# Kernel tuning notes

Hardware: AMD Instinct MI355X
Metric: run time of the kernel (lower is better)

## Reference

```python
import jax, jax.numpy as jnp
import numpy as np

B, N, F, UNITS = 8, 2048, 64, 64

def setup_inputs() -> dict:
    key = jax.random.key(0)
    ks = jax.random.split(key, 7)
    inputs = jax.random.normal(ks[0], (B, N, F), dtype=jnp.float32)
    Dynamic_L = jax.random.normal(ks[1], (B, N, N), dtype=jnp.float32)
    W = jax.random.uniform(ks[2], (B, N, N, 3), dtype=jnp.float32)
    Geo = jax.random.normal(ks[3], (N, N), dtype=jnp.float32)
    KL = jax.random.normal(ks[4], (N, N), dtype=jnp.float32)
    # Dense(Units, tanh) params (glorot-ish scale)
    Wd = jax.random.normal(ks[5], (F, UNITS), dtype=jnp.float32) / np.sqrt(F)
    bd = jnp.zeros((UNITS,), dtype=jnp.float32)
    return {"inputs": inputs, "Dynamic_L": Dynamic_L, "W": W,
            "Geo": Geo, "KL": KL, "Wd": Wd, "bd": bd}

def reference(inputs, Dynamic_L, W, Geo, KL, Wd, bd):
    # Weighted fusion of three N x N matrices; Geo/KL broadcast over batch.
    Fusion = Dynamic_L * W[..., 0] + Geo[None] * W[..., 1] + KL[None] * W[..., 2]  # [B,N,N]
    Fusion = jax.nn.softmax(Fusion, axis=-1)
    G1 = jnp.einsum('bnm,bmf->bnf', Fusion, inputs)  # graph matmul [B,N,F]
    return jnp.tanh(G1 @ Wd + bd)  # Dense(Units, tanh) -> [B,N,UNITS]
```

## Files before the change

### kernel.cpp

```cpp
#include <hip/hip_runtime.h>
#include <hip/hip_fp16.h>

#define Nn 2048
#define Ff 64
#define Uu 64
#define NT 256
#define NCH 4

typedef _Float16 f16x4 __attribute__((ext_vector_type(4)));
typedef _Float16 f16x8 __attribute__((ext_vector_type(8)));
typedef float    f32x4 __attribute__((ext_vector_type(4)));

#define MFMA32(a,b,c) __builtin_amdgcn_mfma_f32_16x16x32_f16(a,b,c,0,0,0)
#define G1S 68

__global__ __launch_bounds__(256) void transposeX(const float* __restrict__ X,
                                                  _Float16* __restrict__ Xt) {
    __shared__ _Float16 tile[64][65];
    const int b = blockIdx.x, kt = blockIdx.y;
    #pragma unroll
    for (int i = 0; i < 16; ++i) {
        int e  = i * 256 + threadIdx.x;
        int kk = e >> 6, ff = e & 63;
        tile[ff][kk] = (_Float16)X[((size_t)b * Nn + kt * 64 + kk) * Ff + ff];
    }
    __syncthreads();
    #pragma unroll
    for (int i = 0; i < 16; ++i) {
        int e  = i * 256 + threadIdx.x;
        int ff = e >> 6, kk = e & 63;
        Xt[((size_t)b * Ff + ff) * Nn + kt * 64 + kk] = tile[ff][kk];
    }
}

#define ISSUE_HR(Vd,Vw0,Vw1,Vw2,Vg,Vk, C, HR) {               \
    const int _rr = (HR) >> 1;                                \
    const int _m  = ((C) << 9) + (((HR) & 1) << 8) + (lane << 2); \
    const size_t _o = (size_t)_rr * Nn + _m;                  \
    Vd  = *(const float4*)(dR + _o);                          \
    Vw0 = *(const float4*)(wR + 3 * _o);                      \
    Vw1 = *(const float4*)(wR + 3 * _o + 4);                  \
    Vw2 = *(const float4*)(wR + 3 * _o + 8);                  \
    Vg  = *(const float4*)(gR + _o);                          \
    Vk  = *(const float4*)(kR + _o);                          \
}

#define CONSUME_HR(Vd,Vw0,Vw1,Vw2,Vg,Vk, BUF, HR) {                           \
    const int _rr = (HR) >> 1;                                                \
    const int _tr = row0 + _rr;                                               \
    float _e0 = __expf(fminf(Vd.x*Vw0.x + Vg.x*Vw0.y + Vk.x*Vw0.z, 11.f));    \
    float _e1 = __expf(fminf(Vd.y*Vw0.w + Vg.y*Vw1.x + Vk.y*Vw1.y, 11.f));    \
    float _e2 = __expf(fminf(Vd.z*Vw1.z + Vg.z*Vw1.w + Vk.z*Vw2.x, 11.f));    \
    float _e3 = __expf(fminf(Vd.w*Vw2.y + Vg.w*Vw2.z + Vk.w*Vw2.w, 11.f));    \
    f16x4 _h = {(_Float16)_e0, (_Float16)_e1, (_Float16)_e2, (_Float16)_e3};  \
    rs[_rr] += (float)_h[0] + (float)_h[1] + (float)_h[2] + (float)_h[3];     \
    const int _ba = _tr*1024 + (((HR)&1) << 9) + (lane << 3);                 \
    *(f16x4*)((char*)(BUF) + (_ba ^ ((_tr & 7) << 4))) = _h;                  \
}

#define STAGE_CHUNK(BUF, C) {                          \
    ISSUE_HR(Ad,Aw0,Aw1,Aw2,Ag,Ak, C, 0);              \
    ISSUE_HR(Bd,Bw0,Bw1,Bw2,Bg,Bk, C, 1);              \
    CONSUME_HR(Ad,Aw0,Aw1,Aw2,Ag,Ak, BUF, 0);          \
    ISSUE_HR(Ad,Aw0,Aw1,Aw2,Ag,Ak, C, 2);              \
    CONSUME_HR(Bd,Bw0,Bw1,Bw2,Bg,Bk, BUF, 1);          \
    ISSUE_HR(Bd,Bw0,Bw1,Bw2,Bg,Bk, C, 3);              \
    CONSUME_HR(Ad,Aw0,Aw1,Aw2,Ag,Ak, BUF, 2);          \
    ISSUE_HR(Ad,Aw0,Aw1,Aw2,Ag,Ak, C, 4);              \
    CONSUME_HR(Bd,Bw0,Bw1,Bw2,Bg,Bk, BUF, 3);          \
    ISSUE_HR(Bd,Bw0,Bw1,Bw2,Bg,Bk, C, 5);              \
    CONSUME_HR(Ad,Aw0,Aw1,Aw2,Ag,Ak, BUF, 4);          \
    ISSUE_HR(Ad,Aw0,Aw1,Aw2,Ag,Ak, C, 6);              \
    CONSUME_HR(Bd,Bw0,Bw1,Bw2,Bg,Bk, BUF, 5);          \
    ISSUE_HR(Bd,Bw0,Bw1,Bw2,Bg,Bk, C, 7);              \
    CONSUME_HR(Ad,Aw0,Aw1,Aw2,Ag,Ak, BUF, 6);          \
    CONSUME_HR(Bd,Bw0,Bw1,Bw2,Bg,Bk, BUF, 7);          \
}

#define MFMA_PHASE(BUFC, XC) {                                                \
    f16x8 p0 = *(const f16x8*)((XC));                                         \
    f16x8 p1 = *(const f16x8*)((XC) + 32);                                    \
    f16x8 p2 = *(const f16x8*)((XC) + 64);                                    \
    f16x8 p3 = *(const f16x8*)((XC) + 96);                                    \
    f16x8 p4 = *(const f16x8*)((XC) + 128);                                   \
    f16x8 p5 = *(const f16x8*)((XC) + 160);                                   \
    f16x8 p6 = *(const f16x8*)((XC) + 192);                                   \
    f16x8 p7 = *(const f16x8*)((XC) + 224);                                   \
    _Pragma("unroll")                                                         \
    for (int kk = 0; kk < 8; ++kk) {                                          \
        const int aa = r * 1024 + kk * 64 + kg * 16;                          \
        f16x8 af = *(const f16x8*)((BUFC) + (aa ^ ((r & 7) << 4)));           \
        f16x8 bv = (kk==0)?p0:(kk==1)?p1:(kk==2)?p2:(kk==3)?p3:               \
                   (kk==4)?p4:(kk==5)?p5:(kk==6)?p6:p7;                       \
        acc = MFMA32(af, bv, acc);                                            \
    }                                                                         \
    p0 = *(const f16x8*)((XC) + 256);                                         \
    p1 = *(const f16x8*)((XC) + 288);                                         \
    p2 = *(const f16x8*)((XC) + 320);                                         \
    p3 = *(const f16x8*)((XC) + 352);                                         \
    p4 = *(const f16x8*)((XC) + 384);                                         \
    p5 = *(const f16x8*)((XC) + 416);                                         \
    p6 = *(const f16x8*)((XC) + 448);                                         \
    p7 = *(const f16x8*)((XC) + 480);                                         \
    _Pragma("unroll")                                                         \
    for (int kk = 0; kk < 8; ++kk) {                                          \
        const int aa = r * 1024 + (kk + 8) * 64 + kg * 16;                    \
        f16x8 af = *(const f16x8*)((BUFC) + (aa ^ ((r & 7) << 4)));           \
        f16x8 bv = (kk==0)?p0:(kk==1)?p1:(kk==2)?p2:(kk==3)?p3:               \
                   (kk==4)?p4:(kk==5)?p5:(kk==6)?p6:p7;                       \
        acc = MFMA32(af, bv, acc);                                            \
    }                                                                         \
}

__global__ __launch_bounds__(NT, 4) void fused_gcn(
    const _Float16* __restrict__ Xt,
    const float* __restrict__ Dyn,
    const float* __restrict__ Wf,
    const float* __restrict__ Geo,
    const float* __restrict__ KLm,
    const float* __restrict__ Wd,
    const float* __restrict__ bdv,
    float* __restrict__ out)
{
    __shared__ _Float16 Pb[2][16 * 512];
    __shared__ float wsumS[16];
    __shared__ float invS[16];

    const int t    = threadIdx.x;
    const int lane = t & 63;
    const int wid  = t >> 6;
    const int r    = lane & 15;
    const int kg   = lane >> 4;
    const int b    = blockIdx.x >> 7;
    const int n0   = (blockIdx.x & 127) << 4;
    const int row0 = wid << 2;

    const float* dR = Dyn + ((size_t)b * Nn + n0 + row0) * Nn;
    const float* wR = Wf  + ((size_t)b * Nn + n0 + row0) * (size_t)Nn * 3;
    const float* gR = Geo + (size_t)(n0 + row0) * Nn;
    const float* kR = KLm + (size_t)(n0 + row0) * Nn;
    const _Float16* XtB = Xt + (size_t)b * Ff * Nn;
    const _Float16* xw  = XtB + (size_t)(wid * 16 + r) * Nn + (kg << 3);

    f32x4 acc = {0.f, 0.f, 0.f, 0.f};
    float rs[4] = {0.f, 0.f, 0.f, 0.f};
    float4 Ad, Aw0, Aw1, Aw2, Ag, Ak;
    float4 Bd, Bw0, Bw1, Bw2, Bg, Bk;

    STAGE_CHUNK(&Pb[0][0], 0);
    __syncthreads();

    #pragma unroll 1
    for (int c = 0; c < NCH; ++c) {
        const char* bufc = (const char*)&Pb[c & 1][0];
        MFMA_PHASE(bufc, xw + (c << 9));
        if (c + 1 < NCH) {
            _Float16* bufn = &Pb[(c + 1) & 1][0];
            STAGE_CHUNK(bufn, c + 1);
        }
        __syncthreads();
    }

    #pragma unroll
    for (int i = 0; i < 4; ++i) {
        float v = rs[i];
        v += __shfl_xor(v, 1, 64);  v += __shfl_xor(v, 2, 64);
        v += __shfl_xor(v, 4, 64);  v += __shfl_xor(v, 8, 64);
        v += __shfl_xor(v, 16, 64); v += __shfl_xor(v, 32, 64);
        rs[i] = v;
    }
    if (lane == 0) {
        wsumS[row0 + 0] = rs[0]; wsumS[row0 + 1] = rs[1];
        wsumS[row0 + 2] = rs[2]; wsumS[row0 + 3] = rs[3];
    }
    __syncthreads();
    if (t < 16) invS[t] = 1.0f / wsumS[t];
    __syncthreads();

    float* g1 = (float*)&Pb[0][0];
    #pragma unroll
    for (int i = 0; i < 4; ++i) {
        const int ro = (kg << 2) + i;
        g1[ro * G1S + (wid << 4) + r] = acc[i] * invS[ro];
    }
    __syncthreads();

    const float* g1r = g1 + row0 * G1S;
    float o0 = bdv[lane], o1 = o0, o2 = o0, o3 = o0;
    #pragma unroll 4
    for (int f = 0; f < Ff; ++f) {
        float wdv = Wd[f * Uu + lane];
        o0 += g1r[f]           * wdv;
        o1 += g1r[G1S + f]     * wdv;
        o2 += g1r[2 * G1S + f] * wdv;
        o3 += g1r[3 * G1S + f] * wdv;
    }
    float oo[4] = {o0, o1, o2, o3};
    #pragma unroll
    for (int i = 0; i < 4; ++i) {
        float x  = fminf(fmaxf(oo[i], -15.f), 15.f);
        float ex = __expf(2.f * x);
        out[((size_t)b * Nn + n0 + row0 + i) * Uu + lane] = (ex - 1.f) / (ex + 1.f);
    }
}

extern "C" void kernel_launch(void* const* d_in, const int* in_sizes, int n_in,
                              void* d_out, int out_size, void* d_ws, size_t ws_size,
                              hipStream_t stream) {
    const float* X   = (const float*)d_in[0];
    const float* Dyn = (const float*)d_in[1];
    const float* Wf  = (const float*)d_in[2];
    const float* Geo = (const float*)d_in[3];
    const float* KLm = (const float*)d_in[4];
    const float* Wd  = (const float*)d_in[5];
    const float* bdv = (const float*)d_in[6];
    float* out = (float*)d_out;

    _Float16* Xt = (_Float16*)d_ws;
    transposeX<<<dim3(8, Nn / 64), dim3(256), 0, stream>>>(X, Xt);
    fused_gcn<<<dim3(8 * (Nn / 16)), dim3(NT), 0, stream>>>(
        Xt, Dyn, Wf, Geo, KLm, Wd, bdv, out);
}
```

Baseline: 129.5 us.

## Warp-specialize fused GCN into producer softmax waves and consumer MFMA waves

Result: slower. 158.7 us (+22.5%).

```diff
diff --git a/kernel.cpp b/kernel.cpp
--- a/kernel.cpp
+++ b/kernel.cpp
@@ -5,7 +5,8 @@
 #define Ff 64
 #define Uu 64
 #define NT 256
-#define NCH 4
+#define CW 256
+#define NCH 8
 
 typedef _Float16 f16x4 __attribute__((ext_vector_type(4)));
 typedef _Float16 f16x8 __attribute__((ext_vector_type(8)));
@@ -33,83 +34,59 @@
     }
 }
 
-#define ISSUE_HR(Vd,Vw0,Vw1,Vw2,Vg,Vk, C, HR) {               \
-    const int _rr = (HR) >> 1;                                \
-    const int _m  = ((C) << 9) + (((HR) & 1) << 8) + (lane << 2); \
-    const size_t _o = (size_t)_rr * Nn + _m;                  \
-    Vd  = *(const float4*)(dR + _o);                          \
-    Vw0 = *(const float4*)(wR + 3 * _o);                      \
-    Vw1 = *(const float4*)(wR + 3 * _o + 4);                  \
-    Vw2 = *(const float4*)(wR + 3 * _o + 8);                  \
-    Vg  = *(const float4*)(gR + _o);                          \
-    Vk  = *(const float4*)(kR + _o);                          \
-}
-
-#define CONSUME_HR(Vd,Vw0,Vw1,Vw2,Vg,Vk, BUF, HR) {                           \
-    const int _rr = (HR) >> 1;                                                \
-    const int _tr = row0 + _rr;                                               \
+#define ISSUE_U(Vd,Vw0,Vw1,Vw2,Vg,Vk, C, U) {                 \
+    const size_t _o = (size_t)(U) * Nn + (size_t)(C) * CW + (lane << 2); \
+    Vd  = *(const float4*)(dP + _o);                          \
+    Vw0 = *(const float4*)(wP + 3 * _o);                      \
+    Vw1 = *(const float4*)(wP + 3 * _o + 4);                  \
+    Vw2 = *(const float4*)(wP + 3 * _o + 8);                  \
+    Vg  = *(const float4*)(gP + _o);                          \
+    Vk  = *(const float4*)(kP + _o);                          \
+}
+
+#define CONSUME_U(Vd,Vw0,Vw1,Vw2,Vg,Vk, BUF, U) {                             \
     float _e0 = __expf(fminf(Vd.x*Vw0.x + Vg.x*Vw0.y + Vk.x*Vw0.z, 11.f));    \
     float _e1 = __expf(fminf(Vd.y*Vw0.w + Vg.y*Vw1.x + Vk.y*Vw1.y, 11.f));    \
     float _e2 = __expf(fminf(Vd.z*Vw1.z + Vg.z*Vw1.w + Vk.z*Vw2.x, 11.f));    \
     float _e3 = __expf(fminf(Vd.w*Vw2.y + Vg.w*Vw2.z + Vk.w*Vw2.w, 11.f));    \
     f16x4 _h = {(_Float16)_e0, (_Float16)_e1, (_Float16)_e2, (_Float16)_e3};  \
-    rs[_rr] += (float)_h[0] + (float)_h[1] + (float)_h[2] + (float)_h[3];     \
-    const int _ba = _tr*1024 + (((HR)&1) << 9) + (lane << 3);                 \
-    *(f16x4*)((char*)(BUF) + (_ba ^ ((_tr & 7) << 4))) = _h;                  \
-}
-
-#define STAGE_CHUNK(BUF, C) {                          \
-    ISSUE_HR(Ad,Aw0,Aw1,Aw2,Ag,Ak, C, 0);              \
-    ISSUE_HR(Bd,Bw0,Bw1,Bw2,Bg,Bk, C, 1);              \
-    CONSUME_HR(Ad,Aw0,Aw1,Aw2,Ag,Ak, BUF, 0);          \
-    ISSUE_HR(Ad,Aw0,Aw1,Aw2,Ag,Ak, C, 2);              \
-    CONSUME_HR(Bd,Bw0,Bw1,Bw2,Bg,Bk, BUF, 1);          \
-    ISSUE_HR(Bd,Bw0,Bw1,Bw2,Bg,Bk, C, 3);              \
-    CONSUME_HR(Ad,Aw0,Aw1,Aw2,Ag,Ak, BUF, 2);          \
-    ISSUE_HR(Ad,Aw0,Aw1,Aw2,Ag,Ak, C, 4);              \
-    CONSUME_HR(Bd,Bw0,Bw1,Bw2,Bg,Bk, BUF, 3);          \
-    ISSUE_HR(Bd,Bw0,Bw1,Bw2,Bg,Bk, C, 5);              \
-    CONSUME_HR(Ad,Aw0,Aw1,Aw2,Ag,Ak, BUF, 4);          \
-    ISSUE_HR(Ad,Aw0,Aw1,Aw2,Ag,Ak, C, 6);              \
-    CONSUME_HR(Bd,Bw0,Bw1,Bw2,Bg,Bk, BUF, 5);          \
-    ISSUE_HR(Bd,Bw0,Bw1,Bw2,Bg,Bk, C, 7);              \
-    CONSUME_HR(Ad,Aw0,Aw1,Aw2,Ag,Ak, BUF, 6);          \
-    CONSUME_HR(Bd,Bw0,Bw1,Bw2,Bg,Bk, BUF, 7);          \
-}
-
-#define MFMA_PHASE(BUFC, XC) {                                                \
-    f16x8 p0 = *(const f16x8*)((XC));                                         \
-    f16x8 p1 = *(const f16x8*)((XC) + 32);                                    \
-    f16x8 p2 = *(const f16x8*)((XC) + 64);                                    \
-    f16x8 p3 = *(const f16x8*)((XC) + 96);                                    \
-    f16x8 p4 = *(const f16x8*)((XC) + 128);                                   \
-    f16x8 p5 = *(const f16x8*)((XC) + 160);                                   \
-    f16x8 p6 = *(const f16x8*)((XC) + 192);                                   \
-    f16x8 p7 = *(const f16x8*)((XC) + 224);                                   \
-    _Pragma("unroll")                                                         \
-    for (int kk = 0; kk < 8; ++kk) {                                          \
-        const int aa = r * 1024 + kk * 64 + kg * 16;                          \
-        f16x8 af = *(const f16x8*)((BUFC) + (aa ^ ((r & 7) << 4)));           \
-        f16x8 bv = (kk==0)?p0:(kk==1)?p1:(kk==2)?p2:(kk==3)?p3:               \
-                   (kk==4)?p4:(kk==5)?p5:(kk==6)?p6:p7;                       \
-        acc = MFMA32(af, bv, acc);                                            \
-    }                                                                         \
-    p0 = *(const f16x8*)((XC) + 256);                                         \
-    p1 = *(const f16x8*)((XC) + 288);                                         \
-    p2 = *(const f16x8*)((XC) + 320);                                         \
-    p3 = *(const f16x8*)((XC) + 352);                                         \
-    p4 = *(const f16x8*)((XC) + 384);                                         \
-    p5 = *(const f16x8*)((XC) + 416);                                         \
-    p6 = *(const f16x8*)((XC) + 448);                                         \
-    p7 = *(const f16x8*)((XC) + 480);                                         \
-    _Pragma("unroll")                                                         \
-    for (int kk = 0; kk < 8; ++kk) {                                          \
-        const int aa = r * 1024 + (kk + 8) * 64 + kg * 16;                    \
-        f16x8 af = *(const f16x8*)((BUFC) + (aa ^ ((r & 7) << 4)));           \
-        f16x8 bv = (kk==0)?p0:(kk==1)?p1:(kk==2)?p2:(kk==3)?p3:               \
-                   (kk==4)?p4:(kk==5)?p5:(kk==6)?p6:p7;                       \
-        acc = MFMA32(af, bv, acc);                                            \
-    }                                                                         \
+    rs[U] += (float)_h[0] + (float)_h[1] + (float)_h[2] + (float)_h[3];       \
+    const int _ba = (p8 + (U)) * 512 + (lane << 3);                           \
+    *(f16x4*)((char*)(BUF) + (_ba ^ (((U) & 7) << 4))) = _h;                  \
+}
+
+#define STAGE_BODY(BUF, C, PRE) {                          \
+    CONSUME_U(Ad,Aw0,Aw1,Aw2,Ag,Ak, BUF, 0);               \
+    ISSUE_U(Ad,Aw0,Aw1,Aw2,Ag,Ak, C, 2);                   \
+    CONSUME_U(Bd,Bw0,Bw1,Bw2,Bg,Bk, BUF, 1);               \
+    ISSUE_U(Bd,Bw0,Bw1,Bw2,Bg,Bk, C, 3);                   \
+    CONSUME_U(Ad,Aw0,Aw1,Aw2,Ag,Ak, BUF, 2);               \
+    ISSUE_U(Ad,Aw0,Aw1,Aw2,Ag,Ak, C, 4);                   \
+    CONSUME_U(Bd,Bw0,Bw1,Bw2,Bg,Bk, BUF, 3);               \
+    ISSUE_U(Bd,Bw0,Bw1,Bw2,Bg,Bk, C, 5);                   \
+    CONSUME_U(Ad,Aw0,Aw1,Aw2,Ag,Ak, BUF, 4);               \
+    ISSUE_U(Ad,Aw0,Aw1,Aw2,Ag,Ak, C, 6);                   \
+    CONSUME_U(Bd,Bw0,Bw1,Bw2,Bg,Bk, BUF, 5);               \
+    ISSUE_U(Bd,Bw0,Bw1,Bw2,Bg,Bk, C, 7);                   \
+    CONSUME_U(Ad,Aw0,Aw1,Aw2,Ag,Ak, BUF, 6);               \
+    if (PRE) { ISSUE_U(Ad,Aw0,Aw1,Aw2,Ag,Ak, (C)+1, 0); }  \
+    CONSUME_U(Bd,Bw0,Bw1,Bw2,Bg,Bk, BUF, 7);               \
+    if (PRE) { ISSUE_U(Bd,Bw0,Bw1,Bw2,Bg,Bk, (C)+1, 1); }  \
+}
+
+#define MFMA_CHUNK(BUF, C) {                                        \
+    const char* _bc = (const char*)(BUF);                           \
+    const _Float16* _x0 = xB0 + (size_t)(C) * CW;                   \
+    const _Float16* _x1 = xB1 + (size_t)(C) * CW;                   \
+    _Pragma("unroll")                                               \
+    for (int kk = 0; kk < 8; ++kk) {                                \
+        const int aa = r * 512 + kk * 64 + kg * 16;                 \
+        f16x8 af = *(const f16x8*)(_bc + (aa ^ ((r & 7) << 4)));    \
+        f16x8 b0 = *(const f16x8*)(_x0 + kk * 32);                  \
+        f16x8 b1 = *(const f16x8*)(_x1 + kk * 32);                  \
+        acc0 = MFMA32(af, b0, acc0);                                \
+        acc1 = MFMA32(af, b1, acc1);                                \
+    }                                                               \
 }
 
 __global__ __launch_bounds__(NT, 4) void fused_gcn(
@@ -122,9 +99,10 @@
     const float* __restrict__ bdv,
     float* __restrict__ out)
 {
-    __shared__ _Float16 Pb[2][16 * 512];
+    __shared__ _Float16 Pb[2][16 * CW];
     __shared__ float wsumS[16];
     __shared__ float invS[16];
+    __shared__ float g1[16 * G1S];
 
     const int t    = threadIdx.x;
     const int lane = t & 63;
@@ -133,58 +111,65 @@
     const int kg   = lane >> 4;
     const int b    = blockIdx.x >> 7;
     const int n0   = (blockIdx.x & 127) << 4;
-    const int row0 = wid << 2;
-
-    const float* dR = Dyn + ((size_t)b * Nn + n0 + row0) * Nn;
-    const float* wR = Wf  + ((size_t)b * Nn + n0 + row0) * (size_t)Nn * 3;
-    const float* gR = Geo + (size_t)(n0 + row0) * Nn;
-    const float* kR = KLm + (size_t)(n0 + row0) * Nn;
-    const _Float16* XtB = Xt + (size_t)b * Ff * Nn;
-    const _Float16* xw  = XtB + (size_t)(wid * 16 + r) * Nn + (kg << 3);
-
-    f32x4 acc = {0.f, 0.f, 0.f, 0.f};
-    float rs[4] = {0.f, 0.f, 0.f, 0.f};
+
+    const int p  = wid & 1;
+    const int p8 = p << 3;
+    const float* dP = Dyn + ((size_t)b * Nn + n0 + p8) * Nn;
+    const float* wP = Wf  + ((size_t)b * Nn + n0 + p8) * (size_t)Nn * 3;
+    const float* gP = Geo + (size_t)(n0 + p8) * Nn;
+    const float* kP = KLm + (size_t)(n0 + p8) * Nn;
+
+    const int cw = wid & 1;
+    const _Float16* xB0 = Xt + (size_t)b * Ff * Nn
+                        + (size_t)((cw * 2) * 16 + r) * Nn + (kg << 3);
+    const _Float16* xB1 = xB0 + (size_t)16 * Nn;
+
+    float rs[8] = {0.f,0.f,0.f,0.f,0.f,0.f,0.f,0.f};
+    f32x4 acc0 = {0.f,0.f,0.f,0.f}, acc1 = {0.f,0.f,0.f,0.f};
     float4 Ad, Aw0, Aw1, Aw2, Ag, Ak;
     float4 Bd, Bw0, Bw1, Bw2, Bg, Bk;
 
-    STAGE_CHUNK(&Pb[0][0], 0);
-    __syncthreads();
+    if (wid < 2) {
+        ISSUE_U(Ad,Aw0,Aw1,Aw2,Ag,Ak, 0, 0);
+        ISSUE_U(Bd,Bw0,Bw1,Bw2,Bg,Bk, 0, 1);
+    }
 
     #pragma unroll 1
-    for (int c = 0; c < NCH; ++c) {
-        const char* bufc = (const char*)&Pb[c & 1][0];
-        MFMA_PHASE(bufc, xw + (c << 9));
-        if (c + 1 < NCH) {
-            _Float16* bufn = &Pb[(c + 1) & 1][0];
-            STAGE_CHUNK(bufn, c + 1);
+    for (int it = 0; it < NCH + 1; ++it) {
+        if (wid < 2) {
+            if (it < NCH) STAGE_BODY(&Pb[it & 1][0], it, (it + 1 < NCH));
+        } else {
+            if (it > 0) MFMA_CHUNK(&Pb[(it - 1) & 1][0], it - 1);
         }
         __syncthreads();
     }
 
-    #pragma unroll
-    for (int i = 0; i < 4; ++i) {
-        float v = rs[i];
-        v += __shfl_xor(v, 1, 64);  v += __shfl_xor(v, 2, 64);
-        v += __shfl_xor(v, 4, 64);  v += __shfl_xor(v, 8, 64);
-        v += __shfl_xor(v, 16, 64); v += __shfl_xor(v, 32, 64);
-        rs[i] = v;
-    }
-    if (lane == 0) {
-        wsumS[row0 + 0] = rs[0]; wsumS[row0 + 1] = rs[1];
-        wsumS[row0 + 2] = rs[2]; wsumS[row0 + 3] = rs[3];
+    if (wid < 2) {
+        #pragma unroll
+        for (int u = 0; u < 8; ++u) {
+            float v = rs[u];
+            v += __shfl_xor(v, 1, 64);  v += __shfl_xor(v, 2, 64);
+            v += __shfl_xor(v, 4, 64);  v += __shfl_xor(v, 8, 64);
+            v += __shfl_xor(v, 16, 64); v += __shfl_xor(v, 32, 64);
+            if (lane == 0) wsumS[p8 + u] = v;
+        }
     }
     __syncthreads();
     if (t < 16) invS[t] = 1.0f / wsumS[t];
     __syncthreads();
 
-    float* g1 = (float*)&Pb[0][0];
-    #pragma unroll
-    for (int i = 0; i < 4; ++i) {
-        const int ro = (kg << 2) + i;
-        g1[ro * G1S + (wid << 4) + r] = acc[i] * invS[ro];
-    }
-    __syncthreads();
-
+    if (wid >= 2) {
+        #pragma unroll
+        for (int i = 0; i < 4; ++i) {
+            const int ro = (kg << 2) + i;
+            const float inv = invS[ro];
+            g1[ro * G1S + (cw * 2) * 16 + r]       = acc0[i] * inv;
+            g1[ro * G1S + (cw * 2 + 1) * 16 + r]   = acc1[i] * inv;
+        }
+    }
+    __syncthreads();
+
+    const int row0 = wid << 2;
     const float* g1r = g1 + row0 * G1S;
     float o0 = bdv[lane], o1 = o0, o2 = o0, o3 = o0;
     #pragma unroll 4
```

## Process two batches per block to share Geo/KL row loads

Applied to the files above, without the earlier changes.

Measured after the change: 130.9 us. About the same (+1.1%).

```diff
diff --git a/kernel.cpp b/kernel.cpp
--- a/kernel.cpp
+++ b/kernel.cpp
@@ -6,13 +6,20 @@
 #define Uu 64
 #define NT 256
 #define NCH 4
+#define G1S 68
 
 typedef _Float16 f16x4 __attribute__((ext_vector_type(4)));
 typedef _Float16 f16x8 __attribute__((ext_vector_type(8)));
 typedef float    f32x4 __attribute__((ext_vector_type(4)));
 
 #define MFMA32(a,b,c) __builtin_amdgcn_mfma_f32_16x16x32_f16(a,b,c,0,0,0)
-#define G1S 68
+
+#define OPB   0
+#define OG1A  65536
+#define OG1B  69888
+#define OWS   74240
+#define OINV  74368
+#define SMSZ  74496
 
 __global__ __launch_bounds__(256) void transposeX(const float* __restrict__ X,
                                                   _Float16* __restrict__ Xt) {
@@ -33,51 +40,63 @@
     }
 }
 
-#define ISSUE_HR(Vd,Vw0,Vw1,Vw2,Vg,Vk, C, HR) {               \
-    const int _rr = (HR) >> 1;                                \
-    const int _m  = ((C) << 9) + (((HR) & 1) << 8) + (lane << 2); \
-    const size_t _o = (size_t)_rr * Nn + _m;                  \
-    Vd  = *(const float4*)(dR + _o);                          \
-    Vw0 = *(const float4*)(wR + 3 * _o);                      \
-    Vw1 = *(const float4*)(wR + 3 * _o + 4);                  \
-    Vw2 = *(const float4*)(wR + 3 * _o + 8);                  \
-    Vg  = *(const float4*)(gR + _o);                          \
-    Vk  = *(const float4*)(kR + _o);                          \
-}
-
-#define CONSUME_HR(Vd,Vw0,Vw1,Vw2,Vg,Vk, BUF, HR) {                           \
-    const int _rr = (HR) >> 1;                                                \
-    const int _tr = row0 + _rr;                                               \
-    float _e0 = __expf(fminf(Vd.x*Vw0.x + Vg.x*Vw0.y + Vk.x*Vw0.z, 11.f));    \
-    float _e1 = __expf(fminf(Vd.y*Vw0.w + Vg.y*Vw1.x + Vk.y*Vw1.y, 11.f));    \
-    float _e2 = __expf(fminf(Vd.z*Vw1.z + Vg.z*Vw1.w + Vk.z*Vw2.x, 11.f));    \
-    float _e3 = __expf(fminf(Vd.w*Vw2.y + Vg.w*Vw2.z + Vk.w*Vw2.w, 11.f));    \
-    f16x4 _h = {(_Float16)_e0, (_Float16)_e1, (_Float16)_e2, (_Float16)_e3};  \
-    rs[_rr] += (float)_h[0] + (float)_h[1] + (float)_h[2] + (float)_h[3];     \
-    const int _ba = _tr*1024 + (((HR)&1) << 9) + (lane << 3);                 \
-    *(f16x4*)((char*)(BUF) + (_ba ^ ((_tr & 7) << 4))) = _h;                  \
-}
-
-#define STAGE_CHUNK(BUF, C) {                          \
-    ISSUE_HR(Ad,Aw0,Aw1,Aw2,Ag,Ak, C, 0);              \
-    ISSUE_HR(Bd,Bw0,Bw1,Bw2,Bg,Bk, C, 1);              \
-    CONSUME_HR(Ad,Aw0,Aw1,Aw2,Ag,Ak, BUF, 0);          \
-    ISSUE_HR(Ad,Aw0,Aw1,Aw2,Ag,Ak, C, 2);              \
-    CONSUME_HR(Bd,Bw0,Bw1,Bw2,Bg,Bk, BUF, 1);          \
-    ISSUE_HR(Bd,Bw0,Bw1,Bw2,Bg,Bk, C, 3);              \
-    CONSUME_HR(Ad,Aw0,Aw1,Aw2,Ag,Ak, BUF, 2);          \
-    ISSUE_HR(Ad,Aw0,Aw1,Aw2,Ag,Ak, C, 4);              \
-    CONSUME_HR(Bd,Bw0,Bw1,Bw2,Bg,Bk, BUF, 3);          \
-    ISSUE_HR(Bd,Bw0,Bw1,Bw2,Bg,Bk, C, 5);              \
-    CONSUME_HR(Ad,Aw0,Aw1,Aw2,Ag,Ak, BUF, 4);          \
-    ISSUE_HR(Ad,Aw0,Aw1,Aw2,Ag,Ak, C, 6);              \
-    CONSUME_HR(Bd,Bw0,Bw1,Bw2,Bg,Bk, BUF, 5);          \
-    ISSUE_HR(Bd,Bw0,Bw1,Bw2,Bg,Bk, C, 7);              \
-    CONSUME_HR(Ad,Aw0,Aw1,Aw2,Ag,Ak, BUF, 6);          \
-    CONSUME_HR(Bd,Bw0,Bw1,Bw2,Bg,Bk, BUF, 7);          \
-}
-
-#define MFMA_PHASE(BUFC, XC) {                                                \
+#define ISSUE2(d0v,d1v,gv,kv,w00,w01,w02,w10,w11,w12, C, HR) {      \
+    const int _rr = (HR) >> 1;                                      \
+    const size_t _o = (size_t)_rr * Nn + ((size_t)(C) << 9)         \
+                    + (((HR) & 1) << 8) + (lane << 2);              \
+    d0v = *(const float4*)(dR0 + _o);                               \
+    d1v = *(const float4*)(dR1 + _o);                               \
+    gv  = *(const float4*)(gR + _o);                                \
+    kv  = *(const float4*)(kR + _o);                                \
+    w00 = *(const float4*)(wR0 + 3 * _o);                           \
+    w01 = *(const float4*)(wR0 + 3 * _o + 4);                       \
+    w02 = *(const float4*)(wR0 + 3 * _o + 8);                       \
+    w10 = *(const float4*)(wR1 + 3 * _o);                           \
+    w11 = *(const float4*)(wR1 + 3 * _o + 4);                       \
+    w12 = *(const float4*)(wR1 + 3 * _o + 8);                       \
+}
+
+#define CONSUME2(d0v,d1v,gv,kv,w00,w01,w02,w10,w11,w12, P0B,P1B, HR) {          \
+    const int _rr = (HR) >> 1;                                                  \
+    const int _tr = row0 + _rr;                                                 \
+    float a0 = __expf(fminf(d0v.x*w00.x + gv.x*w00.y + kv.x*w00.z, 11.f));      \
+    float a1 = __expf(fminf(d0v.y*w00.w + gv.y*w01.x + kv.y*w01.y, 11.f));      \
+    float a2 = __expf(fminf(d0v.z*w01.z + gv.z*w01.w + kv.z*w02.x, 11.f));      \
+    float a3 = __expf(fminf(d0v.w*w02.y + gv.w*w02.z + kv.w*w02.w, 11.f));      \
+    float c0 = __expf(fminf(d1v.x*w10.x + gv.x*w10.y + kv.x*w10.z, 11.f));      \
+    float c1 = __expf(fminf(d1v.y*w10.w + gv.y*w11.x + kv.y*w11.y, 11.f));      \
+    float c2 = __expf(fminf(d1v.z*w11.z + gv.z*w11.w + kv.z*w12.x, 11.f));      \
+    float c3 = __expf(fminf(d1v.w*w12.y + gv.w*w12.z + kv.w*w12.w, 11.f));      \
+    f16x4 h0 = {(_Float16)a0, (_Float16)a1, (_Float16)a2, (_Float16)a3};        \
+    f16x4 h1 = {(_Float16)c0, (_Float16)c1, (_Float16)c2, (_Float16)c3};        \
+    rs0[_rr] += (float)h0[0] + (float)h0[1] + (float)h0[2] + (float)h0[3];      \
+    rs1[_rr] += (float)h1[0] + (float)h1[1] + (float)h1[2] + (float)h1[3];      \
+    const int _ba = (_tr * 1024 + (((HR) & 1) << 9) + (lane << 3))              \
+                    ^ ((_tr & 7) << 4);                                         \
+    *(f16x4*)((P0B) + _ba) = h0;                                                \
+    *(f16x4*)((P1B) + _ba) = h1;                                                \
+}
+
+#define STAGE_CHUNK2(P0B, P1B, C) {                                              \
+    ISSUE2(Ad0,Ad1,Agv,Akv,Aw00,Aw01,Aw02,Aw10,Aw11,Aw12, C, 0);                 \
+    ISSUE2(Bd0,Bd1,Bgv,Bkv,Bw00,Bw01,Bw02,Bw10,Bw11,Bw12, C, 1);                 \
+    CONSUME2(Ad0,Ad1,Agv,Akv,Aw00,Aw01,Aw02,Aw10,Aw11,Aw12, P0B,P1B, 0);         \
+    ISSUE2(Ad0,Ad1,Agv,Akv,Aw00,Aw01,Aw02,Aw10,Aw11,Aw12, C, 2);                 \
+    CONSUME2(Bd0,Bd1,Bgv,Bkv,Bw00,Bw01,Bw02,Bw10,Bw11,Bw12, P0B,P1B, 1);         \
+    ISSUE2(Bd0,Bd1,Bgv,Bkv,Bw00,Bw01,Bw02,Bw10,Bw11,Bw12, C, 3);                 \
+    CONSUME2(Ad0,Ad1,Agv,Akv,Aw00,Aw01,Aw02,Aw10,Aw11,Aw12, P0B,P1B, 2);         \
+    ISSUE2(Ad0,Ad1,Agv,Akv,Aw00,Aw01,Aw02,Aw10,Aw11,Aw12, C, 4);                 \
+    CONSUME2(Bd0,Bd1,Bgv,Bkv,Bw00,Bw01,Bw02,Bw10,Bw11,Bw12, P0B,P1B, 3);         \
+    ISSUE2(Bd0,Bd1,Bgv,Bkv,Bw00,Bw01,Bw02,Bw10,Bw11,Bw12, C, 5);                 \
+    CONSUME2(Ad0,Ad1,Agv,Akv,Aw00,Aw01,Aw02,Aw10,Aw11,Aw12, P0B,P1B, 4);         \
+    ISSUE2(Ad0,Ad1,Agv,Akv,Aw00,Aw01,Aw02,Aw10,Aw11,Aw12, C, 6);                 \
+    CONSUME2(Bd0,Bd1,Bgv,Bkv,Bw00,Bw01,Bw02,Bw10,Bw11,Bw12, P0B,P1B, 5);         \
+    ISSUE2(Bd0,Bd1,Bgv,Bkv,Bw00,Bw01,Bw02,Bw10,Bw11,Bw12, C, 7);                 \
+    CONSUME2(Ad0,Ad1,Agv,Akv,Aw00,Aw01,Aw02,Aw10,Aw11,Aw12, P0B,P1B, 6);         \
+    CONSUME2(Bd0,Bd1,Bgv,Bkv,Bw00,Bw01,Bw02,Bw10,Bw11,Bw12, P0B,P1B, 7);         \
+}
+
+#define MFMA_PHASE2(PBUF, XC, ACC) {                                          \
     f16x8 p0 = *(const f16x8*)((XC));                                         \
     f16x8 p1 = *(const f16x8*)((XC) + 32);                                    \
     f16x8 p2 = *(const f16x8*)((XC) + 64);                                    \
@@ -89,10 +108,10 @@
     _Pragma("unroll")                                                         \
     for (int kk = 0; kk < 8; ++kk) {                                          \
         const int aa = r * 1024 + kk * 64 + kg * 16;                          \
-        f16x8 af = *(const f16x8*)((BUFC) + (aa ^ ((r & 7) << 4)));           \
+        f16x8 af = *(const f16x8*)((PBUF) + (aa ^ ((r & 7) << 4)));           \
         f16x8 bv = (kk==0)?p0:(kk==1)?p1:(kk==2)?p2:(kk==3)?p3:               \
                    (kk==4)?p4:(kk==5)?p5:(kk==6)?p6:p7;                       \
-        acc = MFMA32(af, bv, acc);                                            \
+        ACC = MFMA32(af, bv, ACC);                                            \
     }                                                                         \
     p0 = *(const f16x8*)((XC) + 256);                                         \
     p1 = *(const f16x8*)((XC) + 288);                                         \
@@ -105,14 +124,14 @@
     _Pragma("unroll")                                                         \
     for (int kk = 0; kk < 8; ++kk) {                                          \
         const int aa = r * 1024 + (kk + 8) * 64 + kg * 16;                    \
-        f16x8 af = *(const f16x8*)((BUFC) + (aa ^ ((r & 7) << 4)));           \
+        f16x8 af = *(const f16x8*)((PBUF) + (aa ^ ((r & 7) << 4)));           \
         f16x8 bv = (kk==0)?p0:(kk==1)?p1:(kk==2)?p2:(kk==3)?p3:               \
                    (kk==4)?p4:(kk==5)?p5:(kk==6)?p6:p7;                       \
-        acc = MFMA32(af, bv, acc);                                            \
+        ACC = MFMA32(af, bv, ACC);                                            \
     }                                                                         \
 }
 
-__global__ __launch_bounds__(NT, 4) void fused_gcn(
+__global__ __launch_bounds__(NT, 2) void fused_gcn(
     const _Float16* __restrict__ Xt,
     const float* __restrict__ Dyn,
     const float* __restrict__ Wf,
@@ -122,85 +141,100 @@
     const float* __restrict__ bdv,
     float* __restrict__ out)
 {
-    __shared__ _Float16 Pb[2][16 * 512];
-    __shared__ float wsumS[16];
-    __shared__ float invS[16];
+    __shared__ __align__(16) char SM[SMSZ];
 
     const int t    = threadIdx.x;
     const int lane = t & 63;
     const int wid  = t >> 6;
     const int r    = lane & 15;
     const int kg   = lane >> 4;
-    const int b    = blockIdx.x >> 7;
-    const int n0   = (blockIdx.x & 127) << 4;
+    const int rg   = blockIdx.x & 127;
+    const int pp   = blockIdx.x >> 7;
+    const int n0   = rg << 4;
+    const int b0   = pp * 2, b1 = pp * 2 + 1;
     const int row0 = wid << 2;
 
-    const float* dR = Dyn + ((size_t)b * Nn + n0 + row0) * Nn;
-    const float* wR = Wf  + ((size_t)b * Nn + n0 + row0) * (size_t)Nn * 3;
-    const float* gR = Geo + (size_t)(n0 + row0) * Nn;
-    const float* kR = KLm + (size_t)(n0 + row0) * Nn;
-    const _Float16* XtB = Xt + (size_t)b * Ff * Nn;
-    const _Float16* xw  = XtB + (size_t)(wid * 16 + r) * Nn + (kg << 3);
-
-    f32x4 acc = {0.f, 0.f, 0.f, 0.f};
-    float rs[4] = {0.f, 0.f, 0.f, 0.f};
-    float4 Ad, Aw0, Aw1, Aw2, Ag, Ak;
-    float4 Bd, Bw0, Bw1, Bw2, Bg, Bk;
-
-    STAGE_CHUNK(&Pb[0][0], 0);
+    const float* dR0 = Dyn + ((size_t)b0 * Nn + n0 + row0) * Nn;
+    const float* dR1 = Dyn + ((size_t)b1 * Nn + n0 + row0) * Nn;
+    const float* wR0 = Wf  + ((size_t)b0 * Nn + n0 + row0) * (size_t)Nn * 3;
+    const float* wR1 = Wf  + ((size_t)b1 * Nn + n0 + row0) * (size_t)Nn * 3;
+    const float* gR  = Geo + (size_t)(n0 + row0) * Nn;
+    const float* kR  = KLm + (size_t)(n0 + row0) * Nn;
+    const _Float16* xw0 = Xt + (size_t)b0 * Ff * Nn
+                        + (size_t)(wid * 16 + r) * Nn + (kg << 3);
+    const _Float16* xw1 = Xt + (size_t)b1 * Ff * Nn
+                        + (size_t)(wid * 16 + r) * Nn + (kg << 3);
+
+    f32x4 acc0 = {0.f,0.f,0.f,0.f}, acc1 = {0.f,0.f,0.f,0.f};
+    float rs0[4] = {0.f,0.f,0.f,0.f}, rs1[4] = {0.f,0.f,0.f,0.f};
+    float4 Ad0,Ad1,Agv,Akv,Aw00,Aw01,Aw02,Aw10,Aw11,Aw12;
+    float4 Bd0,Bd1,Bgv,Bkv,Bw00,Bw01,Bw02,Bw10,Bw11,Bw12;
+
+    STAGE_CHUNK2(SM + OPB, SM + OPB + 16384, 0);
     __syncthreads();
 
     #pragma unroll 1
     for (int c = 0; c < NCH; ++c) {
-        const char* bufc = (const char*)&Pb[c & 1][0];
-        MFMA_PHASE(bufc, xw + (c << 9));
+        char* bufc = SM + OPB + (c & 1) * 32768;
+        MFMA_PHASE2(bufc,          xw0 + ((size_t)c << 9), acc0);
+        MFMA_PHASE2(bufc + 16384,  xw1 + ((size_t)c << 9), acc1);
         if (c + 1 < NCH) {
-            _Float16* bufn = &Pb[(c + 1) & 1][0];
-            STAGE_CHUNK(bufn, c + 1);
+            char* bufn = SM + OPB + ((c + 1) & 1) * 32768;
+            STAGE_CHUNK2(bufn, bufn + 16384, c + 1);
         }
         __syncthreads();
     }
 
+    float* ws = (float*)(SM + OWS);
     #pragma unroll
     for (int i = 0; i < 4; ++i) {
-        float v = rs[i];
+        float v = rs0[i];
         v += __shfl_xor(v, 1, 64);  v += __shfl_xor(v, 2, 64);
         v += __shfl_xor(v, 4, 64);  v += __shfl_xor(v, 8, 64);
         v += __shfl_xor(v, 16, 64); v += __shfl_xor(v, 32, 64);
-        rs[i] = v;
-    }
-    if (lane == 0) {
-        wsumS[row0 + 0] = rs[0]; wsumS[row0 + 1] = rs[1];
-        wsumS[row0 + 2] = rs[2]; wsumS[row0 + 3] = rs[3];
-    }
-    __syncthreads();
-    if (t < 16) invS[t] = 1.0f / wsumS[t];
-    __syncthreads();
-
-    float* g1 = (float*)&Pb[0][0];
+        float u = rs1[i];
+        u += __shfl_xor(u, 1, 64);  u += __shfl_xor(u, 2, 64);
+        u += __shfl_xor(u, 4, 64);  u += __shfl_xor(u, 8, 64);
+        u += __shfl_xor(u, 16, 64); u += __shfl_xor(u, 32, 64);
+        if (lane == 0) { ws[row0 + i] = v; ws[16 + row0 + i] = u; }
+    }
+    __syncthreads();
+    float* inv = (float*)(SM + OINV);
+    if (t < 32) inv[t] = 1.0f / ws[t];
+    __syncthreads();
+
+    float* g1a = (float*)(SM + OG1A);
+    float* g1b = (float*)(SM + OG1B);
     #pragma unroll
     for (int i = 0; i < 4; ++i) {
         const int ro = (kg << 2) + i;
-        g1[ro * G1S + (wid << 4) + r] = acc[i] * invS[ro];
-    }
-    __syncthreads();
-
-    const float* g1r = g1 + row0 * G1S;
-    float o0 = bdv[lane], o1 = o0, o2 = o0, o3 = o0;
+        g1a[ro * G1S + (wid << 4) + r] = acc0[i] * inv[ro];
+        g1b[ro * G1S + (wid << 4) + r] = acc1[i] * inv[16 + ro];
+    }
+    __syncthreads();
+
+    const float* ga = g1a + row0 * G1S;
+    const float* gb = g1b + row0 * G1S;
+    float bb = bdv[lane];
+    float a0 = bb, a1 = bb, a2 = bb, a3 = bb;
+    float c0 = bb, c1 = bb, c2 = bb, c3 = bb;
     #pragma unroll 4
     for (int f = 0; f < Ff; ++f) {
         float wdv = Wd[f * Uu + lane];
-        o0 += g1r[f]           * wdv;
-        o1 += g1r[G1S + f]     * wdv;
-        o2 += g1r[2 * G1S + f] * wdv;
-        o3 += g1r[3 * G1S + f] * wdv;
-    }
-    float oo[4] = {o0, o1, o2, o3};
+        a0 += ga[f] * wdv;           a1 += ga[G1S + f] * wdv;
+        a2 += ga[2 * G1S + f] * wdv; a3 += ga[3 * G1S + f] * wdv;
+        c0 += gb[f] * wdv;           c1 += gb[G1S + f] * wdv;
+        c2 += gb[2 * G1S + f] * wdv; c3 += gb[3 * G1S + f] * wdv;
+    }
+    float oa[4] = {a0, a1, a2, a3}, ob[4] = {c0, c1, c2, c3};
     #pragma unroll
     for (int i = 0; i < 4; ++i) {
-        float x  = fminf(fmaxf(oo[i], -15.f), 15.f);
+        float x  = fminf(fmaxf(oa[i], -15.f), 15.f);
         float ex = __expf(2.f * x);
-        out[((size_t)b * Nn + n0 + row0 + i) * Uu + lane] = (ex - 1.f) / (ex + 1.f);
+        out[((size_t)b0 * Nn + n0 + row0 + i) * Uu + lane] = (ex - 1.f) / (ex + 1.f);
+        float y  = fminf(fmaxf(ob[i], -15.f), 15.f);
+        float ey = __expf(2.f * y);
+        out[((size_t)b1 * Nn + n0 + row0 + i) * Uu + lane] = (ey - 1.f) / (ey + 1.f);
     }
 }
 
@@ -218,6 +252,6 @@
 
     _Float16* Xt = (_Float16*)d_ws;
     transposeX<<<dim3(8, Nn / 64), dim3(256), 0, stream>>>(X, Xt);
-    fused_gcn<<<dim3(8 * (Nn / 16)), dim3(NT), 0, stream>>>(
+    fused_gcn<<<dim3(4 * 128), dim3(NT), 0, stream>>>(
         Xt, Dyn, Wf, Geo, KLm, Wd, bdv, out);
 }
```
